# Kernel optimization log

Hardware: AMD Instinct MI355X
Metric: run time of the kernel (lower is better)

## Reference

```python
import jax, jax.numpy as jnp
import numpy as np

WS = 8          # window_size
HEADS = 8
HEAD_DIM = 32
DIM = 256       # input_dim
DISP = WS // 2  # displacement for shifted windows
SCALE = HEAD_DIM ** -0.5
NEG = float('-inf')


def _create_mask(upper_lower, left_right):
    S = WS * WS
    m = np.zeros((S, S), np.float32)
    if upper_lower:
        m[-DISP * WS:, :-DISP * WS] = NEG
        m[:-DISP * WS, -DISP * WS:] = NEG
    if left_right:
        m = m.reshape(WS, WS, WS, WS)
        m[:, -DISP:, :, :-DISP] = NEG
        m[:, :-DISP, :, -DISP:] = NEG
        m = m.reshape(S, S)
    return m


def _shift_mask(nwh, nww):
    # per-window additive mask, [nW, S, S]
    S = WS * WS
    low = _create_mask(True, False)
    right = _create_mask(False, True)
    mask = np.zeros((nwh * nww, S, S), np.float32)
    mask[-nww:] += low                 # bottom row of windows
    mask[nww - 1::nww] += right        # rightmost column of windows
    return mask


def _rel_idx():
    coords = np.array([[x, y] for x in range(WS) for y in range(WS)])
    dist = coords[None, :, :] - coords[:, None, :] + (WS - 1)  # in [0, 2*WS-2]
    return dist[..., 0], dist[..., 1]


def setup_inputs() -> dict:
    key = jax.random.key(0)
    ks = jax.random.split(key, 5)
    B, H, W = 64, 64, 64
    inner = HEADS * HEAD_DIM
    return {
        "x": jax.random.normal(ks[0], (B, H, W, DIM), jnp.float32),
        "qkv_w": jax.random.normal(ks[1], (3 * inner, DIM), jnp.float32) * 0.02,
        "proj_w": jax.random.normal(ks[2], (DIM, inner), jnp.float32) * 0.02,
        "proj_b": jnp.zeros((DIM,), jnp.float32),
        "pos_emb": jax.random.normal(ks[3], (2 * WS - 1, 2 * WS - 1), jnp.float32),
    }


def reference(x, qkv_w, proj_w, proj_b, pos_emb):
    B, H, W, C = x.shape
    nwh, nww = H // WS, W // WS
    nW, S = nwh * nww, WS * WS

    x = jnp.roll(x, (-DISP, -DISP), axis=(1, 2))          # cyclic shift
    qkv = x @ qkv_w.T                                      # [B,H,W,3*inner]
    q, k, v = jnp.split(qkv, 3, axis=-1)

    def towin(t):  # [B,H,W,heads*d] -> [B,heads,nW,S,d]
        t = t.reshape(B, nwh, WS, nww, WS, HEADS, HEAD_DIM)
        return t.transpose(0, 5, 1, 3, 2, 4, 6).reshape(B, HEADS, nW, S, HEAD_DIM)

    q, k, v = towin(q), towin(k), towin(v)

    scores = jnp.einsum('bhwid,bhwjd->bhwij', q, k) * SCALE
    ri, ci = _rel_idx()
    scores = scores + pos_emb[ri, ci]                      # relative position bias [S,S]
    mask = jnp.asarray(_shift_mask(nwh, nww))              # [nW,S,S]
    scores = scores + mask[None, None]

    attn = jax.nn.softmax(scores, axis=-1)
    out = jnp.einsum('bhwij,bhwjd->bhwid', attn, v)        # [B,heads,nW,S,d]

    out = out.reshape(B, HEADS, nwh, nww, WS, WS, HEAD_DIM)
    out = out.transpose(0, 2, 4, 3, 5, 1, 6).reshape(B, H, W, HEADS * HEAD_DIM)

    out = out @ proj_w.T + proj_b
    out = jnp.roll(out, (DISP, DISP), axis=(1, 2))         # reverse cyclic shift
    return out
```

## Files before the change

kernel.cpp:

```cpp
#include <hip/hip_runtime.h>
#include <hip/hip_bf16.h>
#include <math.h>

typedef __bf16 bf16;
typedef bf16 bf16x8 __attribute__((ext_vector_type(8)));
typedef bf16 bf16x4 __attribute__((ext_vector_type(4)));
typedef float f32x4 __attribute__((ext_vector_type(4)));

#define MFMA16(A,B,C) __builtin_amdgcn_mfma_f32_16x16x32_bf16(A,B,C,0,0,0)

static constexpr int QKV_ELEMS  = 768 * 256;
static constexpr int PROJ_ELEMS = 256 * 256;
static constexpr size_t QKVWS_ELEMS = (size_t)4096 * 8 * 6144;

static __device__ __forceinline__ void lds_fence() {
    asm volatile("s_waitcnt lgkmcnt(0)" ::: "memory");
    __builtin_amdgcn_sched_barrier(0);
}

static __device__ __forceinline__ unsigned pack2(float a, float b) {
    bf16 xa = (bf16)a, xb = (bf16)b;
    unsigned short ua, ub;
    __builtin_memcpy(&ua, &xa, 2);
    __builtin_memcpy(&ub, &xb, 2);
    return (unsigned)ua | ((unsigned)ub << 16);
}

#define BUILD_FRAG(dst, PKL0, PKL1, PKH0, PKH1)                               \
  {                                                                            \
    int sA = ((lane & 16) << 1) + lo;                                          \
    int sB = sA + 16;                                                          \
    int a0 = __shfl((int)(PKL0), sA), a1 = __shfl((int)(PKL1), sA);            \
    int a2 = __shfl((int)(PKL0), sB), a3 = __shfl((int)(PKL1), sB);            \
    int b0 = __shfl((int)(PKH0), sA), b1 = __shfl((int)(PKH1), sA);            \
    int b2 = __shfl((int)(PKH0), sB), b3 = __shfl((int)(PKH1), sB);            \
    union { int w[4]; bf16x8 v; } u_;                                          \
    bool uh_ = (lane >= 32);                                                   \
    u_.w[0] = uh_ ? b0 : a0; u_.w[1] = uh_ ? b1 : a1;                          \
    u_.w[2] = uh_ ? b2 : a2; u_.w[3] = uh_ ? b3 : a3;                          \
    dst = u_.v;                                                                \
  }

__global__ void cvt_weights(const float* __restrict__ qkv_w,
                            const float* __restrict__ proj_w,
                            bf16* __restrict__ wq, bf16* __restrict__ wp) {
    int i = blockIdx.x * 256 + threadIdx.x;
    if (i < QKV_ELEMS) wq[i] = (bf16)qkv_w[i];
    int j = i - QKV_ELEMS;
    if (j >= 0 && j < PROJ_ELEMS) wp[j] = (bf16)proj_w[j];
}

__global__ __launch_bounds__(256, 2)
void swin_qkv(const float* __restrict__ x,
              const bf16* __restrict__ wqkv,
              bf16* __restrict__ qkv_ws)
{
    __shared__ alignas(16) unsigned char xbuf[64 * 1024];
    __shared__ alignas(16) unsigned char vtbuf[4][4096];

    const int tid  = threadIdx.x;
    const int wave = tid >> 6, lane = tid & 63;
    const int hi   = lane >> 4, lo = lane & 15;
    const int b    = blockIdx.x >> 6;
    const int w    = blockIdx.x & 63;
    const int wh   = w >> 3, wwi = w & 7;
    const f32x4 zero4 = {0.f, 0.f, 0.f, 0.f};

    #pragma unroll
    for (int i = 0; i < 16; ++i) {
        int tok = wave * 16 + i;
        int gy = ((wh << 3) + (tok >> 3) + 4) & 63;
        int gx = ((wwi << 3) + (tok & 7) + 4) & 63;
        const float* srow = x + (((b << 6) + gy) * 64 + gx) * 256;
        const float* src  = srow + ((lane ^ (tok & 7)) << 2);
        __builtin_amdgcn_global_load_lds(
            (const __attribute__((address_space(1))) unsigned int*)src,
            (__attribute__((address_space(3))) unsigned int*)(xbuf + tok * 1024),
            16, 0, 0);
    }
    asm volatile("s_waitcnt vmcnt(0)" ::: "memory");
    __syncthreads();

    auto ldx = [&](int tok, int c16 ) -> bf16x8 {
        const float4 a = *(const float4*)(xbuf + tok * 1024 + ((c16 ^ (tok & 7)) << 4));
        const float4 c = *(const float4*)(xbuf + tok * 1024 + (((c16 + 1) ^ (tok & 7)) << 4));
        union { unsigned u[4]; bf16x8 v; } r;
        r.u[0] = pack2(a.x, a.y); r.u[1] = pack2(a.z, a.w);
        r.u[2] = pack2(c.x, c.y); r.u[3] = pack2(c.z, c.w);
        return r.v;
    };

    bf16* base0 = qkv_ws + ((size_t)blockIdx.x * 8 + 2 * wave) * 6144;

    #pragma unroll
    for (int pass = 0; pass < 3; ++pass) {
        const int secb = pass * 256 + 64 * wave;

        bf16x8 af[8][4];
        #pragma unroll
        for (int kk = 0; kk < 8; ++kk)
            #pragma unroll
            for (int Mt = 0; Mt < 4; ++Mt)
                af[kk][Mt] = *(const bf16x8*)(wqkv + (secb + 16 * Mt + lo) * 256 + kk * 32 + hi * 8);

        f32x4 acc[4][4];
        #pragma unroll
        for (int Mt = 0; Mt < 4; ++Mt)
            #pragma unroll
            for (int Nt = 0; Nt < 4; ++Nt) acc[Mt][Nt] = zero4;
        #pragma unroll
        for (int kk = 0; kk < 8; ++kk) {
            bf16x8 bx[4];
            #pragma unroll
            for (int Nt = 0; Nt < 4; ++Nt)
                bx[Nt] = ldx(Nt * 16 + lo, 8 * kk + 2 * hi);
            #pragma unroll
            for (int Mt = 0; Mt < 4; ++Mt)
                #pragma unroll
                for (int Nt = 0; Nt < 4; ++Nt)
                    acc[Mt][Nt] = MFMA16(af[kk][Mt], bx[Nt], acc[Mt][Nt]);
        }

        if (pass < 2) {
            #pragma unroll
            for (int Mt = 0; Mt < 4; ++Mt) {
                bf16* hb = base0 + (Mt >> 1) * 6144 + pass * 2048;
                int d0 = ((Mt & 1) << 4) + 4 * hi;
                #pragma unroll
                for (int Nt = 0; Nt < 4; ++Nt) {
                    int tok = Nt * 16 + lo;
                    bf16x4 v;
                    #pragma unroll
                    for (int r = 0; r < 4; ++r) v[r] = (bf16)acc[Mt][Nt][r];
                    *(bf16x4*)(hb + tok * 32 + d0) = v;
                }
            }
        } else {
            unsigned char* vt = vtbuf[wave];
            #pragma unroll
            for (int hh = 0; hh < 2; ++hh) {
                #pragma unroll
                for (int m = 0; m < 2; ++m) {
                    int Mt = 2 * hh + m;
                    #pragma unroll
                    for (int Nt = 0; Nt < 4; ++Nt) {
                        int tok = Nt * 16 + lo;
                        #pragma unroll
                        for (int r = 0; r < 4; ++r) {
                            int d = (m << 4) + 4 * hi + r;
                            int byte = d * 128 + ((2 * tok) ^ (hi << 5));
                            *(bf16*)(vt + byte) = (bf16)acc[Mt][Nt][r];
                        }
                    }
                }
                lds_fence();
                bf16* hb = base0 + hh * 6144 + 4096;
                #pragma unroll
                for (int i = 0; i < 4; ++i) {
                    int d    = lane >> 1;
                    int tok0 = ((lane & 1) << 3) + (i << 4);
                    int byte = d * 128 + ((2 * tok0) ^ (((d >> 2) & 3) << 5));
                    bf16x8 vv = *(const bf16x8*)(vt + byte);
                    *(bf16x8*)(hb + d * 64 + tok0) = vv;
                }
                lds_fence();
            }
        }
    }
}

__global__ __launch_bounds__(256, 2)
void swin_attn_proj(const bf16* __restrict__ qkv_ws,
                    const bf16* __restrict__ wproj,
                    const float* __restrict__ proj_b,
                    const float* __restrict__ pose_g,
                    float* __restrict__ out)
{
    __shared__ alignas(16) unsigned char xbuf[64 * 512];
    __shared__ float pose[225];

    const int tid  = threadIdx.x;
    const int wave = tid >> 6, lane = tid & 63;
    const int hi   = lane >> 4, lo = lane & 15;
    const int b    = blockIdx.x >> 6;
    const int w    = blockIdx.x & 63;
    const int wh   = w >> 3, wwi = w & 7;
    const bool mlow = (wh == 7), mright = (wwi == 7);
    const f32x4 zero4 = {0.f, 0.f, 0.f, 0.f};

    if (tid < 225) pose[tid] = pose_g[tid];
    __syncthreads();

    const bool colmask_ = mright && (((lo & 7) >= 4) != (hi & 1));

    bf16x8 fr[2][12];
    {
        const bf16* b0 = qkv_ws + ((size_t)blockIdx.x * 8 + 2 * wave) * 6144;
        #pragma unroll
        for (int hp = 0; hp < 2; ++hp) {
            const bf16* bb = b0 + hp * 6144;
            #pragma unroll
            for (int i = 0; i < 4; ++i) {
                fr[hp][i]     = *(const bf16x8*)(bb + 2048 + (16 * i + lo) * 32 + hi * 8);
                fr[hp][4 + i] = *(const bf16x8*)(bb + (16 * i + lo) * 32 + hi * 8);
                fr[hp][8 + i] = *(const bf16x8*)(bb + 4096 + (16 * (i & 1) + lo) * 64 + (i >> 1) * 32 + hi * 8);
            }
        }
    }

    #pragma unroll
    for (int hp = 0; hp < 2; ++hp) {
        const int h = 2 * wave + hp;

        #pragma unroll
        for (int it = 0; it < 4; ++it) {
            f32x4 s4[4];
            #pragma unroll
            for (int jt = 0; jt < 4; ++jt) s4[jt] = MFMA16(fr[hp][jt], fr[hp][4 + it], zero4);

            float mx = -INFINITY;
            #pragma unroll
            for (int jt = 0; jt < 4; ++jt) {
                bool tilemask = mlow && ((it >= 2) != (jt >= 2));
                #pragma unroll
                for (int r = 0; r < 4; ++r) {
                    int drow = 2 * jt + (hi >> 1) - 2 * it - (lo >> 3) + 7;
                    int dcol = 4 * (hi & 1) + r - (lo & 7) + 7;
                    float s = s4[jt][r] * 0.17677669529663687f + pose[drow * 15 + dcol];
                    if (tilemask | colmask_) s = -INFINITY;
                    s4[jt][r] = s;
                    mx = fmaxf(mx, s);
                }
            }
            mx = fmaxf(mx, __shfl_xor(mx, 16));
            mx = fmaxf(mx, __shfl_xor(mx, 32));
            float sum = 0.f;
            #pragma unroll
            for (int jt = 0; jt < 4; ++jt)
                #pragma unroll
                for (int r = 0; r < 4; ++r) {
                    float e = __expf(s4[jt][r] - mx);
                    s4[jt][r] = e; sum += e;
                }
            sum += __shfl_xor(sum, 16);
            sum += __shfl_xor(sum, 32);
            float riv = 1.0f / sum;

            unsigned pk[4][2];
            #pragma unroll
            for (int jt = 0; jt < 4; ++jt)
                #pragma unroll
                for (int p = 0; p < 2; ++p)
                    pk[jt][p] = pack2(s4[jt][2 * p], s4[jt][2 * p + 1]);

            f32x4 o2[2] = {zero4, zero4};
            #pragma unroll
            for (int ks = 0; ks < 2; ++ks) {
                bf16x8 pB;
                BUILD_FRAG(pB, pk[2 * ks][0], pk[2 * ks][1], pk[2 * ks + 1][0], pk[2 * ks + 1][1]);
                #pragma unroll
                for (int dMt = 0; dMt < 2; ++dMt)
                    o2[dMt] = MFMA16(fr[hp][8 + ks * 2 + dMt], pB, o2[dMt]);
            }
            #pragma unroll
            for (int dMt = 0; dMt < 2; ++dMt) {
                int tok = it * 16 + lo;
                bf16x4 v;
                #pragma unroll
                for (int r = 0; r < 4; ++r) v[r] = (bf16)(o2[dMt][r] * riv);
                int chunk = ((h << 2) + (dMt << 1) + (hi >> 1)) ^ (tok & 7);
                *(bf16x4*)(xbuf + tok * 512 + (chunk << 4) + ((hi & 1) << 3)) = v;
            }
        }
    }
    __syncthreads();

    bf16x8 bB[8][4];
    #pragma unroll
    for (int kk = 0; kk < 8; ++kk)
        #pragma unroll
        for (int nt = 0; nt < 4; ++nt) {
            int c = wave * 64 + nt * 16 + lo;
            bB[kk][nt] = *(const bf16x8*)(wproj + c * 256 + kk * 32 + hi * 8);
        }

    f32x4 pacc[4][4];
    #pragma unroll
    for (int Mt = 0; Mt < 4; ++Mt)
        #pragma unroll
        for (int nt = 0; nt < 4; ++nt) pacc[Mt][nt] = zero4;
    #pragma unroll
    for (int kk = 0; kk < 8; ++kk) {
        bf16x8 aA[4];
        #pragma unroll
        for (int Mt = 0; Mt < 4; ++Mt) {
            int tok = Mt * 16 + lo;
            aA[Mt] = *(const bf16x8*)(xbuf + tok * 512 + (((kk * 4 + hi) ^ (tok & 7)) << 4));
        }
        #pragma unroll
        for (int Mt = 0; Mt < 4; ++Mt)
            #pragma unroll
            for (int nt = 0; nt < 4; ++nt)
                pacc[Mt][nt] = MFMA16(aA[Mt], bB[kk][nt], pacc[Mt][nt]);
    }
    #pragma unroll
    for (int nt = 0; nt < 4; ++nt) {
        int c = wave * 64 + nt * 16 + lo;
        float pb2 = proj_b[c];
        #pragma unroll
        for (int Mt = 0; Mt < 4; ++Mt)
            #pragma unroll
            for (int r = 0; r < 4; ++r) {
                int tok = Mt * 16 + 4 * hi + r;
                int fy = ((wh << 3) + (tok >> 3) + 4) & 63;
                int fx = ((wwi << 3) + (tok & 7) + 4) & 63;
                out[(((b << 6) + fy) * 64 + fx) * 256 + c] = pacc[Mt][nt][r] + pb2;
            }
    }
}

extern "C" void kernel_launch(void* const* d_in, const int* in_sizes, int n_in,
                              void* d_out, int out_size, void* d_ws, size_t ws_size,
                              hipStream_t stream) {
    const float* x       = (const float*)d_in[0];
    const float* qkv_w   = (const float*)d_in[1];
    const float* proj_w  = (const float*)d_in[2];
    const float* proj_b  = (const float*)d_in[3];
    const float* pos_emb = (const float*)d_in[4];

    bf16* wq = (bf16*)d_ws;
    bf16* wp = wq + QKV_ELEMS;
    bf16* qkv_ws = wp + PROJ_ELEMS;

    cvt_weights<<<dim3((QKV_ELEMS + PROJ_ELEMS) / 256), dim3(256), 0, stream>>>(
        qkv_w, proj_w, wq, wp);
    swin_qkv<<<dim3(64 * 64), dim3(256), 0, stream>>>(x, wq, qkv_ws);
    swin_attn_proj<<<dim3(64 * 64), dim3(256), 0, stream>>>(
        qkv_ws, wp, proj_b, pos_emb, (float*)d_out);
}
```

Baseline: 446.5 us.

## Read input tile directly from global memory instead of staging in LDS

Removes the 64KB LDS staging buffer for the shifted-window input tile. MFMA B-fragments are now loaded and converted to bf16 straight from global memory, and the weight fragment preload is split into two halves to reduce register pressure. The goal is to free LDS so occupancy can rise and to drop the staging barrier. The cost is that each wave rereads x from global/L2 once per pass (three passes times four waves), where before it was loaded once per block.

```diff
diff --git a/kernel.cpp b/kernel.cpp
--- a/kernel.cpp
+++ b/kernel.cpp
@@ -55,7 +55,6 @@
               const bf16* __restrict__ wqkv,
               bf16* __restrict__ qkv_ws)
 {
-    __shared__ alignas(16) unsigned char xbuf[64 * 1024];
     __shared__ alignas(16) unsigned char vtbuf[4][4096];
 
     const int tid  = threadIdx.x;
@@ -66,29 +65,14 @@
     const int wh   = w >> 3, wwi = w & 7;
     const f32x4 zero4 = {0.f, 0.f, 0.f, 0.f};
 
-    #pragma unroll
-    for (int i = 0; i < 16; ++i) {
-        int tok = wave * 16 + i;
+    const float* xrow[4];
+    #pragma unroll
+    for (int Nt = 0; Nt < 4; ++Nt) {
+        int tok = Nt * 16 + lo;
         int gy = ((wh << 3) + (tok >> 3) + 4) & 63;
         int gx = ((wwi << 3) + (tok & 7) + 4) & 63;
-        const float* srow = x + (((b << 6) + gy) * 64 + gx) * 256;
-        const float* src  = srow + ((lane ^ (tok & 7)) << 2);
-        __builtin_amdgcn_global_load_lds(
-            (const __attribute__((address_space(1))) unsigned int*)src,
-            (__attribute__((address_space(3))) unsigned int*)(xbuf + tok * 1024),
-            16, 0, 0);
-    }
-    asm volatile("s_waitcnt vmcnt(0)" ::: "memory");
-    __syncthreads();
-
-    auto ldx = [&](int tok, int c16 ) -> bf16x8 {
-        const float4 a = *(const float4*)(xbuf + tok * 1024 + ((c16 ^ (tok & 7)) << 4));
-        const float4 c = *(const float4*)(xbuf + tok * 1024 + (((c16 + 1) ^ (tok & 7)) << 4));
-        union { unsigned u[4]; bf16x8 v; } r;
-        r.u[0] = pack2(a.x, a.y); r.u[1] = pack2(a.z, a.w);
-        r.u[2] = pack2(c.x, c.y); r.u[3] = pack2(c.z, c.w);
-        return r.v;
-    };
+        xrow[Nt] = x + (((b << 6) + gy) * 64 + gx) * 256;
+    }
 
     bf16* base0 = qkv_ws + ((size_t)blockIdx.x * 8 + 2 * wave) * 6144;
 
@@ -96,29 +80,40 @@
     for (int pass = 0; pass < 3; ++pass) {
         const int secb = pass * 256 + 64 * wave;
 
-        bf16x8 af[8][4];
-        #pragma unroll
-        for (int kk = 0; kk < 8; ++kk)
-            #pragma unroll
-            for (int Mt = 0; Mt < 4; ++Mt)
-                af[kk][Mt] = *(const bf16x8*)(wqkv + (secb + 16 * Mt + lo) * 256 + kk * 32 + hi * 8);
-
         f32x4 acc[4][4];
         #pragma unroll
         for (int Mt = 0; Mt < 4; ++Mt)
             #pragma unroll
             for (int Nt = 0; Nt < 4; ++Nt) acc[Mt][Nt] = zero4;
-        #pragma unroll
-        for (int kk = 0; kk < 8; ++kk) {
-            bf16x8 bx[4];
-            #pragma unroll
-            for (int Nt = 0; Nt < 4; ++Nt)
-                bx[Nt] = ldx(Nt * 16 + lo, 8 * kk + 2 * hi);
-            #pragma unroll
-            for (int Mt = 0; Mt < 4; ++Mt)
-                #pragma unroll
-                for (int Nt = 0; Nt < 4; ++Nt)
-                    acc[Mt][Nt] = MFMA16(af[kk][Mt], bx[Nt], acc[Mt][Nt]);
+
+        #pragma unroll
+        for (int half = 0; half < 2; ++half) {
+            bf16x8 af[4][4];
+            #pragma unroll
+            for (int k4 = 0; k4 < 4; ++k4)
+                #pragma unroll
+                for (int Mt = 0; Mt < 4; ++Mt)
+                    af[k4][Mt] = *(const bf16x8*)(wqkv + (secb + 16 * Mt + lo) * 256
+                                                  + (half * 4 + k4) * 32 + hi * 8);
+            #pragma unroll
+            for (int k4 = 0; k4 < 4; ++k4) {
+                const int kk = half * 4 + k4;
+                bf16x8 bx[4];
+                #pragma unroll
+                for (int Nt = 0; Nt < 4; ++Nt) {
+                    const float4 a = *(const float4*)(xrow[Nt] + kk * 32 + hi * 8);
+                    const float4 c = *(const float4*)(xrow[Nt] + kk * 32 + hi * 8 + 4);
+                    union { unsigned u[4]; bf16x8 v; } r;
+                    r.u[0] = pack2(a.x, a.y); r.u[1] = pack2(a.z, a.w);
+                    r.u[2] = pack2(c.x, c.y); r.u[3] = pack2(c.z, c.w);
+                    bx[Nt] = r.v;
+                }
+                #pragma unroll
+                for (int Mt = 0; Mt < 4; ++Mt)
+                    #pragma unroll
+                    for (int Nt = 0; Nt < 4; ++Nt)
+                        acc[Mt][Nt] = MFMA16(af[k4][Mt], bx[Nt], acc[Mt][Nt]);
+            }
         }
 
         if (pass < 2) {
```

New measurement: 739.7 us. 65.7% more time.
